# Optimization experiments

Hardware: AMD Instinct MI355X
Metric: run time of the kernel (lower is better)

## Reference

```python
import jax, jax.numpy as jnp
import numpy as np

PI = float(np.pi)
BN_EPS = 1e-3
LN_EPS = 1e-5


def ssslu(x, shape, bias):
    # x * (sin(softsign(x) * shape*pi/2) + (bias + 1))
    s = x / (1.0 + jnp.abs(x))
    return x * (jnp.sin(s * (shape * PI / 2.0)) + (bias + 1.0))


def bn(x, g, b, m, v):
    inv = (g / jnp.sqrt(v + BN_EPS))[None, :, None, None]
    return (x - m[None, :, None, None]) * inv + b[None, :, None, None]


def conv2d(x, w, bias=None, pad=0):
    y = jax.lax.conv_general_dilated(x, w, (1, 1), [(pad, pad), (pad, pad)],
                                     dimension_numbers=('NCHW', 'OIHW', 'NCHW'))
    if bias is not None:
        y = y + bias[None, :, None, None]
    return y


def ln_silu(v):
    # LayerNorm (unit weight, zero bias) over last axis, then SiLU
    mu = jnp.mean(v, axis=-1, keepdims=True)
    var = jnp.mean(jnp.square(v - mu), axis=-1, keepdims=True)
    h = (v - mu) / jnp.sqrt(var + LN_EPS)
    return h * jax.nn.sigmoid(h)


def _forward(x, w_qkv, g_qkv, b_qkv, m_qkv, v_qkv,
             w_co, g_co, b_co, m_co, v_co,
             w_b1, bias_b1, g_b1, b_b1, m_b1, v_b1,
             w_b2, bias_b2, g_b2, b_b2, m_b2, v_b2):
    B, C, H, W = x.shape
    Q = (w_qkv.shape[0] - C) // 2
    # qkv Conv block: conv1x1 -> SSSLU(-3, 0.3) -> BN
    t = bn(ssslu(conv2d(x, w_qkv, pad=0), -3.0, 0.3), g_qkv, b_qkv, m_qkv, v_qkv)
    xq, xk, xv = jnp.split(t, [Q, 2 * Q], axis=1)
    # max-pooled Q/K rows and columns -> [B*Q, W] / [B*Q, H]
    qw = jnp.max(xq, axis=2).reshape(B * Q, W)
    kw = jnp.max(xk, axis=2).reshape(B * Q, W)
    qh = jnp.max(xq, axis=3).reshape(B * Q, H)
    kh = jnp.max(xk, axis=3).reshape(B * Q, H)
    # xaw[i,b] = max_a qw[i,a]*kw[i,b]; xah[i,a] = max_b qh[i,a]*kh[i,b]
    xaw = jnp.max(qw[:, :, None] * kw[:, None, :], axis=1)  # [BQ, W]
    xah = jnp.max(qh[:, :, None] * kh[:, None, :], axis=2)  # [BQ, H]
    xaw = ln_silu(xaw)
    xah = ln_silu(xah)
    xa = (xah[:, :, None] * xaw[:, None, :]).reshape(B, Q, H, W)
    # co: SSSLUConv(Q+C -> Q): conv3x3 -> BN -> SSSLU(1.0, 0)
    xa = jnp.concatenate([xa, xv], axis=1)
    xa = ssslu(bn(conv2d(xa, w_co, pad=1), g_co, b_co, m_co, v_co), 1.0, 0.0)
    # back[0]: Conv(Q -> C, k3, bias): conv -> SSSLU(-3, 0.3) -> BN
    xa = bn(ssslu(conv2d(xa, w_b1, bias_b1, pad=1), -3.0, 0.3), g_b1, b_b1, m_b1, v_b1)
    # back[1]: SSSLUConv(C -> C, k1, bias): conv -> BN -> SSSLU(0.8, 0)
    xa = ssslu(bn(conv2d(xa, w_b2, bias_b2, pad=0), g_b2, b_b2, m_b2, v_b2), 0.8, 0.0)
    # back[2]: Sigmoid; source returns the gate itself
    return jax.nn.sigmoid(xa)


def setup_inputs() -> dict:
    B, C, Q, H, W = 16, 256, 256, 64, 64
    key = jax.random.key(0)
    ks = jax.random.split(key, 32)

    def w_init(k, o, i, kh, kw):
        return jax.random.normal(k, (o, i, kh, kw), jnp.float32) * (1.0 / np.sqrt(i * kh * kw))

    def bn_params(k, c):
        k1, k2, k3, k4 = jax.random.split(k, 4)
        g = jax.random.uniform(k1, (c,), jnp.float32, 0.5, 1.5)
        b = jax.random.normal(k2, (c,), jnp.float32) * 0.1
        m = jax.random.normal(k3, (c,), jnp.float32) * 0.1
        v = jax.random.uniform(k4, (c,), jnp.float32, 0.5, 1.5)
        return g, b, m, v

    x = jax.random.normal(ks[0], (B, C, H, W), jnp.float32)
    w_qkv = w_init(ks[1], 2 * Q + C, C, 1, 1)
    g_qkv, b_qkv, m_qkv, v_qkv = bn_params(ks[2], 2 * Q + C)
    w_co = w_init(ks[3], Q, Q + C, 3, 3)
    g_co, b_co, m_co, v_co = bn_params(ks[4], Q)
    w_b1 = w_init(ks[5], C, Q, 3, 3)
    bias_b1 = jax.random.normal(ks[6], (C,), jnp.float32) * 0.05
    g_b1, b_b1, m_b1, v_b1 = bn_params(ks[7], C)
    w_b2 = w_init(ks[8], C, C, 1, 1)
    bias_b2 = jax.random.normal(ks[9], (C,), jnp.float32) * 0.05
    g_b2, b_b2, m_b2, v_b2 = bn_params(ks[10], C)
    return dict(x=x, w_qkv=w_qkv, g_qkv=g_qkv, b_qkv=b_qkv, m_qkv=m_qkv, v_qkv=v_qkv,
                w_co=w_co, g_co=g_co, b_co=b_co, m_co=m_co, v_co=v_co,
                w_b1=w_b1, bias_b1=bias_b1, g_b1=g_b1, b_b1=b_b1, m_b1=m_b1, v_b1=v_b1,
                w_b2=w_b2, bias_b2=bias_b2, g_b2=g_b2, b_b2=b_b2, m_b2=m_b2, v_b2=v_b2)


def reference(x, w_qkv, g_qkv, b_qkv, m_qkv, v_qkv,
              w_co, g_co, b_co, m_co, v_co,
              w_b1, bias_b1, g_b1, b_b1, m_b1, v_b1,
              w_b2, bias_b2, g_b2, b_b2, m_b2, v_b2):
    return _forward(x, w_qkv, g_qkv, b_qkv, m_qkv, v_qkv,
                    w_co, g_co, b_co, m_co, v_co,
                    w_b1, bias_b1, g_b1, b_b1, m_b1, v_b1,
                    w_b2, bias_b2, g_b2, b_b2, m_b2, v_b2)
```

## Files before the change

kernel.cpp:

```cpp
#include <hip/hip_runtime.h>
#include <hip/hip_bf16.h>
#include <math.h>

#define PI_F 3.14159265358979323846f

typedef unsigned short u16;
typedef unsigned int   u32;
typedef float    f32x4 __attribute__((ext_vector_type(4)));
typedef _Float16 f16x8 __attribute__((ext_vector_type(8)));
typedef u16      u16x8 __attribute__((ext_vector_type(8)));
typedef u16      u16x4 __attribute__((ext_vector_type(4)));

__device__ __forceinline__ u16 f2h(float f){ union{ _Float16 h; u16 u; } c; c.h = (_Float16)f; return c.u; }
__device__ __forceinline__ float h2f(u16 u){ union{ u16 u; _Float16 h; } c; c.u = u; return (float)c.h; }

__device__ __forceinline__ void gl16(const void* g, void* l){
  __builtin_amdgcn_global_load_lds((const __attribute__((address_space(1))) u32*)g,
                                   (__attribute__((address_space(3))) u32*)l, 16, 0, 0);
}

__device__ __forceinline__ int SWZ(int r){ return (r>>1)&3; }

__device__ __forceinline__ float wred_max(float v){
#pragma unroll
  for (int m = 32; m; m >>= 1) v = fmaxf(v, __shfl_xor(v, m));
  return v;
}
__device__ __forceinline__ float wred_min(float v){
#pragma unroll
  for (int m = 32; m; m >>= 1) v = fminf(v, __shfl_xor(v, m));
  return v;
}
__device__ __forceinline__ float wred_sum(float v){
#pragma unroll
  for (int m = 32; m; m >>= 1) v += __shfl_xor(v, m);
  return v;
}

__device__ __forceinline__ float ssslu_f(float x, float shp, float bp1){
  float s = x / (1.0f + fabsf(x));
  return x * (__sinf(s * shp) + bp1);
}

__device__ __forceinline__ float epi_val(float v, float4 p, float shp, float bp1, int ORDER, bool SIG){
  v += p.w;
  if (ORDER == 0){ v = ssslu_f(v, shp, bp1); v = (v - p.z) * p.x + p.y; }
  else           { v = (v - p.z) * p.x + p.y; v = ssslu_f(v, shp, bp1); }
  if (SIG) v = 1.f / (1.f + __expf(-v));
  return v;
}

__device__ __forceinline__ f16x8 mul8h(u16x8 a, u16x8 b){
  union{ u16x8 u; f16x8 h; } A, B; A.u = a; B.u = b;
  return A.h * B.h;
}

__global__ __launch_bounds__(256)
void xpose_k(const float* __restrict__ X, u16* __restrict__ XH)
{
  __shared__ u16 L[16384];
  const int tid = threadIdx.x;
  const int b = blockIdx.x >> 6, h = blockIdx.x & 63;
  const float* xp = X + (size_t)b * 256 * 4096 + h * 64;
#pragma unroll
  for (int i = 0; i < 16; ++i){
    int ci = i * 16 + (tid >> 4);
    int w4 = (tid & 15) * 4;
    float4 v = *(const float4*)(xp + (size_t)ci * 4096 + w4);
    int sw = 4 * ((ci >> 3) & 15);
    u16x4 d;
    d[0] = f2h(v.x); d[1] = f2h(v.y); d[2] = f2h(v.z); d[3] = f2h(v.w);
    *(u16x4*)&L[ci * 64 + (w4 ^ sw)] = d;
  }
  __syncthreads();
  u16* out = XH + (((size_t)b * 4096 + (size_t)h * 64) << 8);
#pragma unroll
  for (int it = 0; it < 8; ++it){
    int w   = it * 8 + (tid >> 5);
    int m   = tid & 31;
    int ci0 = m * 8;
    int base = (w & ~3) ^ (4 * (m & 15));
    int wl   = w & 3;
    u16x8 o;
#pragma unroll
    for (int k = 0; k < 8; ++k)
      o[k] = L[(ci0 + k) * 64 + base + wl];
    *(u16x8*)&out[w * 256 + ci0] = o;
  }
}

template<int CI_T, bool CAT>
__global__ __launch_bounds__(256, 2)
void conv3_mfma(const u16* __restrict__ Apk, const u16* __restrict__ Bg,
                u16* __restrict__ DstH, const float4* __restrict__ pp,
                const u16* __restrict__ xahT_, const u16* __restrict__ xawT_,
                float shp, float bp1, int ORDER)
{
  constexpr int NCC = CI_T / 32;
  constexpr int NIT = NCC * 3;
  __shared__ __align__(16) u16 sAB[37248];

  const int tid  = threadIdx.x;
  const int lane = tid & 63;
  const int wv   = tid >> 6;
  const int wn   = wv;
  const int l15  = lane & 15, l4 = lane >> 4;

  const int bx  = blockIdx.x;
  const int bid = (bx & 7) * 32 + (bx >> 3);
  const int b   = bid >> 4;
  const int r0  = (bid & 15) * 4;
  const int m0  = blockIdx.y * 128;

  if (tid < 192){
    int rr = tid >> 5, rem = tid & 31;
    int wp = (rem & 16) ? 65 : 0;
    *(u32*)&sAB[24576 + rr * 2112 + wp * 32 + (rem & 15) * 2] = 0;
  }
  if (r0 == 0)
    for (int i = tid; i < 1056; i += 256) *(u32*)&sAB[24576 + i * 2] = 0;
  if (r0 == 60)
    for (int i = tid; i < 1056; i += 256) *(u32*)&sAB[24576 + 5 * 2112 + i * 2] = 0;

  const int rA = tid >> 2, s4 = tid & 3;
  const u32 offA0 = ((u32)rA * CI_T + ((s4 ^ SWZ(rA)) << 3)) * 2;
  const u32 offA1 = ((u32)(rA + 64) * CI_T + ((s4 ^ SWZ(rA + 64)) << 3)) * 2;
  const u32 offB  = (((u32)rA << 8) + ((s4 ^ SWZ(rA + 1)) << 3)) * 2;

  auto STAGE_A = [&](int it2){
    int d2 = it2 % 3, c2 = it2 / 3;
    u16* dst = &sAB[(it2 & 1) * 12288 + wv * 512];
    const char* pa = (const char*)(Apk + ((size_t)(d2 * 3 * 256) + m0) * CI_T + c2 * 32);
#pragma unroll
    for (int j2 = 0; j2 < 3; ++j2){
      gl16(pa + offA0, dst + j2 * 4096);
      gl16(pa + offA1, dst + j2 * 4096 + 2048);
      pa += (size_t)256 * CI_T * 2;
    }
  };
  auto STAGE_B = [&](int c2){
#pragma unroll
    for (int j = 0; j < 6; ++j){
      int hh = r0 - 1 + j;
      if ((unsigned)hh >= 64u) continue;
      if (CAT && c2 < 8){
        int w = rA, s = s4;
        int ci0 = c2 * 32 + ((s ^ SWZ(w + 1)) << 3);
        u16x8 vh = *(const u16x8*)&xahT_[((b * 64 + hh) << 8) + ci0];
        u16x8 vw = *(const u16x8*)&xawT_[((b * 64 + w ) << 8) + ci0];
        *(f16x8*)&sAB[24576 + j * 2112 + (w + 1) * 32 + s * 8] = mul8h(vh, vw);
      } else {
        int cio = CAT ? (c2 * 32 - 256) : (c2 * 32);
        const char* pb = (const char*)(Bg + (((size_t)b * 4096 + (size_t)hh * 64) << 8) + cio);
        gl16(pb + offB, &sAB[24576 + j * 2112 + 32 + wv * 512]);
      }
    }
  };

  f32x4 acc[8][4];
#pragma unroll
  for (int i = 0; i < 8; ++i)
#pragma unroll
    for (int j = 0; j < 4; ++j){ acc[i][j][0]=0.f; acc[i][j][1]=0.f; acc[i][j][2]=0.f; acc[i][j][3]=0.f; }

  const char* lds = (const char*)sAB;
  const u32 aoff = (u32)l15 * 64 + (u32)((l4 ^ ((l15 >> 1) & 3)) << 4);
  const char* ab0 = lds + aoff;
  const char* ab1 = lds + aoff + 24576;
  const u32 bcom = 49152u + (u32)wn * 4224;
  const char* bb0 = lds + bcom + (u32)(l15 + 0) * 64 + (u32)((l4 ^ (((l15 + 0) >> 1) & 3)) << 4);
  const char* bb1 = lds + bcom + (u32)(l15 + 1) * 64 + (u32)((l4 ^ (((l15 + 1) >> 1) & 3)) << 4);
  const char* bb2 = lds + bcom + (u32)(l15 + 2) * 64 + (u32)((l4 ^ (((l15 + 2) >> 1) & 3)) << 4);

  STAGE_A(0);

  for (int c = 0; c < NCC; ++c){
#pragma unroll
    for (int d = 0; d < 3; ++d){
      const int it = 3 * c + d;
      if (it + 1 < NIT) STAGE_A(it + 1);
      if (d == 0){ STAGE_B(c); __syncthreads(); }

      const char* ab = ((c + d) & 1) ? ab1 : ab0;
#pragma unroll
      for (int dw = 0; dw < 3; ++dw){
        const char* bp = (dw == 0) ? bb0 : (dw == 1) ? bb1 : bb2;
        f16x8 afr[8], bfr[4];
#pragma unroll
        for (int fm = 0; fm < 8; ++fm)
          afr[fm] = *(const f16x8*)(ab + dw * 8192 + fm * 1024);
#pragma unroll
        for (int fn = 0; fn < 4; ++fn)
          bfr[fn] = *(const f16x8*)(bp + d * 4224 + fn * 1024);
        __builtin_amdgcn_s_setprio(1);
#pragma unroll
        for (int fm = 0; fm < 8; ++fm)
#pragma unroll
          for (int fn = 0; fn < 4; ++fn)
            acc[fm][fn] = __builtin_amdgcn_mfma_f32_16x16x32_f16(afr[fm], bfr[fn], acc[fm][fn], 0, 0, 0);
        __builtin_amdgcn_s_setprio(0);
      }
      __syncthreads();
    }
  }

  const int h = r0 + wn;
#pragma unroll
  for (int fm = 0; fm < 8; ++fm){
    const int cobase = m0 + fm * 16 + 4 * l4;
    float4 P0 = pp[cobase], P1 = pp[cobase+1], P2 = pp[cobase+2], P3 = pp[cobase+3];
#pragma unroll
    for (int fn = 0; fn < 4; ++fn){
      int w = fn * 16 + l15;
      float v0 = epi_val(acc[fm][fn][0], P0, shp, bp1, ORDER, false);
      float v1 = epi_val(acc[fm][fn][1], P1, shp, bp1, ORDER, false);
      float v2 = epi_val(acc[fm][fn][2], P2, shp, bp1, ORDER, false);
      float v3 = epi_val(acc[fm][fn][3], P3, shp, bp1, ORDER, false);
      uint2 st;
      st.x = (u32)f2h(v0) | ((u32)f2h(v1) << 16);
      st.y = (u32)f2h(v2) | ((u32)f2h(v3) << 16);
      *(uint2*)&DstH[(((size_t)b * 4096 + (size_t)h * 64 + w) << 8) + cobase] = st;
    }
  }
}

template<int EPI>
__global__ __launch_bounds__(512, 2)
void conv1_big(const u16* __restrict__ Apk, const u16* __restrict__ Bg,
               u16* __restrict__ DstH, float* __restrict__ DstF,
               const float4* __restrict__ pp,
               float shp, float bp1, int ORDER)
{
  __shared__ __align__(16) u16 sA[2][8192];
  __shared__ __align__(16) u16 sB[2][8192];

  const int tid  = threadIdx.x;
  const int lane = tid & 63;
  const int wv   = tid >> 6;
  const int wm   = wv >> 2;
  const int wn   = wv & 3;
  const int l15  = lane & 15, l4 = lane >> 4;

  const int bx  = blockIdx.x;
  const int bid = (bx & 7) * 32 + (bx >> 3);
  const int b   = bid >> 4;
  const int h0  = (bid & 15) * 4;

  auto STAGE = [&](int c){
    int buf = c & 1;
#pragma unroll
    for (int j = 0; j < 2; ++j){
      int g = j * 512 + tid;
      int m = g >> 2, s = g & 3;
      const u16* srcA = Apk + (size_t)m * 256 + c * 32 + ((s ^ SWZ(m)) << 3);
      gl16(srcA, &sA[buf][(j * 512 + wv * 64) * 8]);
      int r = g >> 8, w = (g >> 2) & 63;
      const u16* srcB = Bg + (((size_t)b * 4096 + (h0 + r) * 64 + w) << 8) + c * 32 + ((s ^ SWZ(w)) << 3);
      gl16(srcB, &sB[buf][(j * 512 + wv * 64) * 8]);
    }
  };

  f32x4 acc[8][4];
#pragma unroll
  for (int i = 0; i < 8; ++i)
#pragma unroll
    for (int j = 0; j < 4; ++j){ acc[i][j][0]=0.f; acc[i][j][1]=0.f; acc[i][j][2]=0.f; acc[i][j][3]=0.f; }

  STAGE(0);
  __syncthreads();

  for (int c = 0; c < 8; ++c){
    if (c + 1 < 8) STAGE(c + 1);
    const int buf = c & 1;
    f16x8 afr[8], bfr[4];
#pragma unroll
    for (int fm = 0; fm < 8; ++fm){
      int m  = wm * 128 + fm * 16 + l15;
      int sl = l4 ^ SWZ(m);
      afr[fm] = *(const f16x8*)&sA[buf][m * 32 + sl * 8];
    }
#pragma unroll
    for (int fn = 0; fn < 4; ++fn){
      int w  = fn * 16 + l15;
      int sl = l4 ^ SWZ(w);
      bfr[fn] = *(const f16x8*)&sB[buf][(wn * 64 + w) * 32 + sl * 8];
    }
    __builtin_amdgcn_s_setprio(1);
#pragma unroll
    for (int fm = 0; fm < 8; ++fm)
#pragma unroll
      for (int fn = 0; fn < 4; ++fn)
        acc[fm][fn] = __builtin_amdgcn_mfma_f32_16x16x32_f16(afr[fm], bfr[fn], acc[fm][fn], 0, 0, 0);
    __builtin_amdgcn_s_setprio(0);
    __syncthreads();
  }

  const int h = h0 + wn;
#pragma unroll
  for (int fm = 0; fm < 8; ++fm){
    const int cobase = wm * 128 + fm * 16 + 4 * l4;
    float4 P0 = pp[cobase], P1 = pp[cobase+1], P2 = pp[cobase+2], P3 = pp[cobase+3];
#pragma unroll
    for (int fn = 0; fn < 4; ++fn){
      int w = fn * 16 + l15;
      if (EPI == 1){
        float v0 = epi_val(acc[fm][fn][0], P0, shp, bp1, ORDER, false);
        float v1 = epi_val(acc[fm][fn][1], P1, shp, bp1, ORDER, false);
        float v2 = epi_val(acc[fm][fn][2], P2, shp, bp1, ORDER, false);
        float v3 = epi_val(acc[fm][fn][3], P3, shp, bp1, ORDER, false);
        uint2 st;
        st.x = (u32)f2h(v0) | ((u32)f2h(v1) << 16);
        st.y = (u32)f2h(v2) | ((u32)f2h(v3) << 16);
        *(uint2*)&DstH[(((size_t)b * 4096 + (size_t)h * 64 + w) << 8) + cobase] = st;
      } else {
        float v0 = epi_val(acc[fm][fn][0], P0, shp, bp1, ORDER, true);
        float v1 = epi_val(acc[fm][fn][1], P1, shp, bp1, ORDER, true);
        float v2 = epi_val(acc[fm][fn][2], P2, shp, bp1, ORDER, true);
        float v3 = epi_val(acc[fm][fn][3], P3, shp, bp1, ORDER, true);
        size_t base = ((size_t)(b * 256 + cobase)) * 4096 + (size_t)h * 64 + w;
        DstF[base]          = v0;
        DstF[base + 4096]   = v1;
        DstF[base + 2*4096] = v2;
        DstF[base + 3*4096] = v3;
      }
    }
  }
}

__global__ __launch_bounds__(512, 2)
void conv1_pool(const u16* __restrict__ Apk0, const u16* __restrict__ Bg,
                const float4* __restrict__ pp0,
                float* __restrict__ qhp, float* __restrict__ khp,
                float* __restrict__ qwp, float* __restrict__ kwp,
                float shp, float bp1)
{
  __shared__ __align__(16) u16 S[32768];
  u16*   sA   = S;
  u16*   sB   = S + 16384;
  float* pool = (float*)S;

  const int tid  = threadIdx.x;
  const int lane = tid & 63;
  const int wv   = tid >> 6;
  const int wm   = wv >> 2;
  const int wn   = wv & 3;
  const int l15  = lane & 15, l4 = lane >> 4;

  const int bx   = blockIdx.x;
  const int bid  = (bx & 7) * 32 + (bx >> 3);
  const int b    = bid >> 4;
  const int hblk = bid & 15;
  const int h0   = hblk * 4;
  const int m0   = blockIdx.y * 256;

  const u16*    Apk = Apk0 + (size_t)m0 * 256;
  const float4* pp  = pp0 + m0;
  float* rowp = (blockIdx.y == 0) ? qhp : khp;
  float* colp = (blockIdx.y == 0) ? qwp : kwp;

  auto STAGE = [&](int c){
    int buf = c & 1;
#pragma unroll
    for (int j = 0; j < 2; ++j){
      int g = j * 512 + tid;
      int m = g >> 2, s = g & 3;
      const u16* srcA = Apk + (size_t)m * 256 + c * 32 + ((s ^ SWZ(m)) << 3);
      gl16(srcA, &sA[buf * 8192 + (j * 512 + wv * 64) * 8]);
      int r = g >> 8, w = (g >> 2) & 63;
      const u16* srcB = Bg + (((size_t)b * 4096 + (h0 + r) * 64 + w) << 8) + c * 32 + ((s ^ SWZ(w)) << 3);
      gl16(srcB, &sB[buf * 8192 + (j * 512 + wv * 64) * 8]);
    }
  };

  f32x4 acc[8][4];
#pragma unroll
  for (int i = 0; i < 8; ++i)
#pragma unroll
    for (int j = 0; j < 4; ++j){ acc[i][j][0]=0.f; acc[i][j][1]=0.f; acc[i][j][2]=0.f; acc[i][j][3]=0.f; }

  STAGE(0);
  __syncthreads();

  for (int c = 0; c < 8; ++c){
    if (c + 1 < 8) STAGE(c + 1);
    const int buf = c & 1;
    f16x8 afr[8], bfr[4];
#pragma unroll
    for (int fm = 0; fm < 8; ++fm){
      int m  = wm * 128 + fm * 16 + l15;
      int sl = l4 ^ SWZ(m);
      afr[fm] = *(const f16x8*)&sA[buf * 8192 + m * 32 + sl * 8];
    }
#pragma unroll
    for (int fn = 0; fn < 4; ++fn){
      int w  = fn * 16 + l15;
      int sl = l4 ^ SWZ(w);
      bfr[fn] = *(const f16x8*)&sB[buf * 8192 + (wn * 64 + w) * 32 + sl * 8];
    }
    __builtin_amdgcn_s_setprio(1);
#pragma unroll
    for (int fm = 0; fm < 8; ++fm)
#pragma unroll
      for (int fn = 0; fn < 4; ++fn)
        acc[fm][fn] = __builtin_amdgcn_mfma_f32_16x16x32_f16(afr[fm], bfr[fn], acc[fm][fn], 0, 0, 0);
    __builtin_amdgcn_s_setprio(0);
    __syncthreads();
  }

  const int h = h0 + wn;
#pragma unroll
  for (int k = 0; k < 4; ++k){
    if (wn == k){
#pragma unroll
      for (int fm = 0; fm < 8; ++fm){
        const int cl = wm * 128 + fm * 16 + 4 * l4;
        float4 P0 = pp[cl], P1 = pp[cl+1], P2 = pp[cl+2], P3 = pp[cl+3];
        float ev[4][4];
#pragma unroll
        for (int fn = 0; fn < 4; ++fn){
          ev[fn][0] = epi_val(acc[fm][fn][0], P0, shp, bp1, 0, false);
          ev[fn][1] = epi_val(acc[fm][fn][1], P1, shp, bp1, 0, false);
          ev[fn][2] = epi_val(acc[fm][fn][2], P2, shp, bp1, 0, false);
          ev[fn][3] = epi_val(acc[fm][fn][3], P3, shp, bp1, 0, false);
        }
#pragma unroll
        for (int r = 0; r < 4; ++r){
          float mv = fmaxf(fmaxf(ev[0][r], ev[1][r]), fmaxf(ev[2][r], ev[3][r]));
          mv = fmaxf(mv, __shfl_xor(mv, 1));
          mv = fmaxf(mv, __shfl_xor(mv, 2));
          mv = fmaxf(mv, __shfl_xor(mv, 4));
          mv = fmaxf(mv, __shfl_xor(mv, 8));
          if (l15 == 0)
            rowp[(((b << 8) | (cl + r)) << 6) + h] = mv;
        }
#pragma unroll
        for (int fn = 0; fn < 4; ++fn)
#pragma unroll
          for (int r = 0; r < 4; ++r){
            int idx = ((cl + r) << 6) + fn * 16 + l15;
            pool[idx] = (k == 0) ? ev[fn][r] : fmaxf(pool[idx], ev[fn][r]);
          }
      }
    }
    __syncthreads();
  }
  float* cbase = colp + (((size_t)(b * 16 + hblk)) << 14);
#pragma unroll
  for (int j = 0; j < 8; ++j){
    int fi = j * 512 + tid;
    *(float4*)&cbase[fi * 4] = *(const float4*)&pool[fi * 4];
  }
}

__device__ __forceinline__ float ln_silu_wave(float v){
  float mu = wred_sum(v) * (1.f / 64.f);
  float d = v - mu;
  float var = wred_sum(d * d) * (1.f / 64.f);
  float hn = d * rsqrtf(var + 1e-5f);
  return hn / (1.f + __expf(-hn));
}

__global__ void attn_k(const float* __restrict__ qwp, const float* __restrict__ kwp,
                       const float* __restrict__ qh, const float* __restrict__ kh,
                       u16* __restrict__ xahT, u16* __restrict__ xawT)
{
  int row  = blockIdx.x * 4 + (threadIdx.x >> 6);
  int lane = threadIdx.x & 63;
  int idx  = (row << 6) + lane;
  int b = row >> 8, q = row & 255;
  size_t pb = ((size_t)b << 18) + (q << 6) + lane;
  float qwv = -3.0e38f, kwv = -3.0e38f;
#pragma unroll
  for (int hb = 0; hb < 16; ++hb){
    qwv = fmaxf(qwv, qwp[pb + ((size_t)hb << 14)]);
    kwv = fmaxf(kwv, kwp[pb + ((size_t)hb << 14)]);
  }
  float qhv = qh[idx], khv = kh[idx];
  float Pq = wred_max(qwv), mq = wred_min(qwv);
  float Pk = wred_max(khv), mk = wred_min(khv);
  float aw = fmaxf(kwv * Pq, kwv * mq);
  float ah = fmaxf(qhv * Pk, qhv * mk);
  aw = ln_silu_wave(aw);
  ah = ln_silu_wave(ah);
  xawT[((b * 64 + lane) << 8) + q] = f2h(aw);
  xahT[((b * 64 + lane) << 8) + q] = f2h(ah);
}

__global__ void pack_k(const float* __restrict__ wqkv, const float* __restrict__ wco,
                       const float* __restrict__ wb1, const float* __restrict__ wb2,
                       const float* gq, const float* bq, const float* mq, const float* vq,
                       const float* gc, const float* bc, const float* mc, const float* vc,
                       const float* g1, const float* b1, const float* m1, const float* v1, const float* bias1,
                       const float* g2, const float* b2, const float* m2, const float* v2, const float* bias2,
                       u16* __restrict__ WQ, u16* __restrict__ WCO, u16* __restrict__ WB1, u16* __restrict__ WB2,
                       float4* __restrict__ PP)
{
  const int E0 = 196608, E1 = 196608 + 1179648, E2 = 196608 + 1179648 + 589824, E3 = 2031616;
  int i = blockIdx.x * 256 + threadIdx.x;
  if (i >= E3 + 1536) return;
  if (i < E0){ WQ[i] = f2h(wqkv[i]); }
  else if (i < E1){
    int d = i - E0; int tap = d / 131072; int rm = d % 131072; int m = rm >> 9; int ci = rm & 511;
    WCO[d] = f2h(wco[(size_t)((m << 9) | ci) * 9 + tap]);
  } else if (i < E2){
    int d = i - E1; int tap = d / 65536; int rm = d & 65535; int m = rm >> 8; int ci = rm & 255;
    WB1[d] = f2h(wb1[(size_t)((m << 8) | ci) * 9 + tap]);
  } else if (i < E3){
    int d = i - E2; WB2[d] = f2h(wb2[d]);
  } else {
    int c = i - E3;
    float g, be, mm, vv, bi;
    if (c < 768){ g = gq[c]; be = bq[c]; mm = mq[c]; vv = vq[c]; bi = 0.f; }
    else if (c < 1024){ int j = c - 768;  g = gc[j]; be = bc[j]; mm = mc[j]; vv = vc[j]; bi = 0.f; }
    else if (c < 1280){ int j = c - 1024; g = g1[j]; be = b1[j]; mm = m1[j]; vv = v1[j]; bi = bias1[j]; }
    else              { int j = c - 1280; g = g2[j]; be = b2[j]; mm = m2[j]; vv = v2[j]; bi = bias2[j]; }
    PP[c] = make_float4(g / sqrtf(vv + 1e-3f), be, mm, bi);
  }
}

extern "C" void kernel_launch(void* const* d_in, const int* in_sizes, int n_in,
                              void* d_out, int out_size, void* d_ws, size_t ws_size,
                              hipStream_t stream)
{
  const float* x       = (const float*)d_in[0];
  const float* w_qkv   = (const float*)d_in[1];
  const float* g_qkv   = (const float*)d_in[2];
  const float* b_qkv   = (const float*)d_in[3];
  const float* m_qkv   = (const float*)d_in[4];
  const float* v_qkv   = (const float*)d_in[5];
  const float* w_co    = (const float*)d_in[6];
  const float* g_co    = (const float*)d_in[7];
  const float* b_co    = (const float*)d_in[8];
  const float* m_co    = (const float*)d_in[9];
  const float* v_co    = (const float*)d_in[10];
  const float* w_b1    = (const float*)d_in[11];
  const float* bias_b1 = (const float*)d_in[12];
  const float* g_b1    = (const float*)d_in[13];
  const float* b_b1    = (const float*)d_in[14];
  const float* m_b1    = (const float*)d_in[15];
  const float* v_b1    = (const float*)d_in[16];
  const float* w_b2    = (const float*)d_in[17];
  const float* bias_b2 = (const float*)d_in[18];
  const float* g_b2    = (const float*)d_in[19];
  const float* b_b2    = (const float*)d_in[20];
  const float* m_b2    = (const float*)d_in[21];
  const float* v_b2    = (const float*)d_in[22];
  float* out = (float*)d_out;

  char* W = (char*)d_ws;
  u16*    WQ   = (u16*)(W + 0);
  u16*    WCO  = (u16*)(W + 393216);
  u16*    WB1  = (u16*)(W + 2752512);
  u16*    WB2  = (u16*)(W + 3932160);
  float4* PP   = (float4*)(W + 4063232);
  float*  qwp_ = (float*)(W + 4087808);
  float*  kwp_ = (float*)(W + 20865024);
  u16*    TV   = (u16*)(W + 4087808);
  u16*    XAHT = (u16*)(W + 37642240);
  u16*    XAWT = (u16*)(W + 38166528);
  u16*    XH   = (u16*)(W + 38690816);
  u16*    Y1   = (u16*)(W + 38690816);
  u16*    Y2   = TV;
  float*  qh_  = (float*)(W + 72245248);
  float*  kh_  = (float*)(W + 73293824);

  const size_t NEED = 74342400;
  if (ws_size < NEED) return;

  const float SHP_N3 = -3.0f * PI_F * 0.5f;
  const float SHP_1  =  1.0f * PI_F * 0.5f;
  const float SHP_08 =  0.8f * PI_F * 0.5f;

  dim3 blk(256);

  pack_k<<<7942, blk, 0, stream>>>(w_qkv, w_co, w_b1, w_b2,
      g_qkv, b_qkv, m_qkv, v_qkv,
      g_co,  b_co,  m_co,  v_co,
      g_b1,  b_b1,  m_b1,  v_b1,  bias_b1,
      g_b2,  b_b2,  m_b2,  v_b2,  bias_b2,
      WQ, WCO, WB1, WB2, PP);

  xpose_k<<<1024, blk, 0, stream>>>(x, XH);

  conv1_pool<<<dim3(256, 2), 512, 0, stream>>>(
      WQ, XH, PP, qh_, kh_, qwp_, kwp_, SHP_N3, 1.3f);

  attn_k<<<1024, blk, 0, stream>>>(qwp_, kwp_, qh_, kh_, XAHT, XAWT);

  conv1_big<1><<<256, 512, 0, stream>>>(
      WQ + (size_t)512 * 256, XH, TV, nullptr, PP + 512, SHP_N3, 1.3f, 0);

  conv3_mfma<512, true><<<dim3(256, 2), blk, 0, stream>>>(
      WCO, TV, Y1, PP + 768, XAHT, XAWT, SHP_1, 1.0f, 1);

  conv3_mfma<256, false><<<dim3(256, 2), blk, 0, stream>>>(
      WB1, Y1, Y2, PP + 1024, nullptr, nullptr, SHP_N3, 1.3f, 0);

  conv1_big<2><<<256, 512, 0, stream>>>(
      WB2, Y2, nullptr, out, PP + 1280, SHP_08, 1.0f, 1);
}
```

Baseline: 433.8 us.

## Keep full weight tile resident in LDS and stream activations straight to registers

Merges the 1x1-conv GEMM kernels into one templated kernel. It loads the whole 256x256 weight slice into 128KB of LDS once, up front, and reads activation fragments directly from global memory into registers with one-step prefetch. This removes the per-chunk double-buffered LDS staging and the per-iteration barriers. In exchange, LDS use rises to 128KB, which likely cuts occupancy to one block per CU, and B reads from global are uncoalesced fragment loads.

```diff
diff --git a/kernel.cpp b/kernel.cpp
--- a/kernel.cpp
+++ b/kernel.cpp
@@ -226,13 +226,15 @@
 
 template<int EPI>
 __global__ __launch_bounds__(512, 2)
-void conv1_big(const u16* __restrict__ Apk, const u16* __restrict__ Bg,
+void conv1_res(const u16* __restrict__ Apk0, const u16* __restrict__ Bg,
                u16* __restrict__ DstH, float* __restrict__ DstF,
-               const float4* __restrict__ pp,
+               const float4* __restrict__ pp0,
+               float* __restrict__ qhp, float* __restrict__ khp,
+               float* __restrict__ qwp, float* __restrict__ kwp,
                float shp, float bp1, int ORDER)
 {
-  __shared__ __align__(16) u16 sA[2][8192];
-  __shared__ __align__(16) u16 sB[2][8192];
+  __shared__ __align__(16) u16 AL[65536];
+  float* pool = (float*)AL;
 
   const int tid  = threadIdx.x;
   const int lane = tid & 63;
@@ -241,136 +243,33 @@
   const int wn   = wv & 3;
   const int l15  = lane & 15, l4 = lane >> 4;
 
-  const int bx  = blockIdx.x;
-  const int bid = (bx & 7) * 32 + (bx >> 3);
-  const int b   = bid >> 4;
-  const int h0  = (bid & 15) * 4;
-
-  auto STAGE = [&](int c){
-    int buf = c & 1;
-#pragma unroll
-    for (int j = 0; j < 2; ++j){
-      int g = j * 512 + tid;
-      int m = g >> 2, s = g & 3;
-      const u16* srcA = Apk + (size_t)m * 256 + c * 32 + ((s ^ SWZ(m)) << 3);
-      gl16(srcA, &sA[buf][(j * 512 + wv * 64) * 8]);
-      int r = g >> 8, w = (g >> 2) & 63;
-      const u16* srcB = Bg + (((size_t)b * 4096 + (h0 + r) * 64 + w) << 8) + c * 32 + ((s ^ SWZ(w)) << 3);
-      gl16(srcB, &sB[buf][(j * 512 + wv * 64) * 8]);
-    }
-  };
-
-  f32x4 acc[8][4];
-#pragma unroll
-  for (int i = 0; i < 8; ++i)
-#pragma unroll
-    for (int j = 0; j < 4; ++j){ acc[i][j][0]=0.f; acc[i][j][1]=0.f; acc[i][j][2]=0.f; acc[i][j][3]=0.f; }
-
-  STAGE(0);
-  __syncthreads();
-
-  for (int c = 0; c < 8; ++c){
-    if (c + 1 < 8) STAGE(c + 1);
-    const int buf = c & 1;
-    f16x8 afr[8], bfr[4];
-#pragma unroll
-    for (int fm = 0; fm < 8; ++fm){
-      int m  = wm * 128 + fm * 16 + l15;
-      int sl = l4 ^ SWZ(m);
-      afr[fm] = *(const f16x8*)&sA[buf][m * 32 + sl * 8];
-    }
-#pragma unroll
-    for (int fn = 0; fn < 4; ++fn){
-      int w  = fn * 16 + l15;
-      int sl = l4 ^ SWZ(w);
-      bfr[fn] = *(const f16x8*)&sB[buf][(wn * 64 + w) * 32 + sl * 8];
-    }
-    __builtin_amdgcn_s_setprio(1);
-#pragma unroll
-    for (int fm = 0; fm < 8; ++fm)
-#pragma unroll
-      for (int fn = 0; fn < 4; ++fn)
-        acc[fm][fn] = __builtin_amdgcn_mfma_f32_16x16x32_f16(afr[fm], bfr[fn], acc[fm][fn], 0, 0, 0);
-    __builtin_amdgcn_s_setprio(0);
-    __syncthreads();
-  }
-
-  const int h = h0 + wn;
-#pragma unroll
-  for (int fm = 0; fm < 8; ++fm){
-    const int cobase = wm * 128 + fm * 16 + 4 * l4;
-    float4 P0 = pp[cobase], P1 = pp[cobase+1], P2 = pp[cobase+2], P3 = pp[cobase+3];
-#pragma unroll
-    for (int fn = 0; fn < 4; ++fn){
-      int w = fn * 16 + l15;
-      if (EPI == 1){
-        float v0 = epi_val(acc[fm][fn][0], P0, shp, bp1, ORDER, false);
-        float v1 = epi_val(acc[fm][fn][1], P1, shp, bp1, ORDER, false);
-        float v2 = epi_val(acc[fm][fn][2], P2, shp, bp1, ORDER, false);
-        float v3 = epi_val(acc[fm][fn][3], P3, shp, bp1, ORDER, false);
-        uint2 st;
-        st.x = (u32)f2h(v0) | ((u32)f2h(v1) << 16);
-        st.y = (u32)f2h(v2) | ((u32)f2h(v3) << 16);
-        *(uint2*)&DstH[(((size_t)b * 4096 + (size_t)h * 64 + w) << 8) + cobase] = st;
-      } else {
-        float v0 = epi_val(acc[fm][fn][0], P0, shp, bp1, ORDER, true);
-        float v1 = epi_val(acc[fm][fn][1], P1, shp, bp1, ORDER, true);
-        float v2 = epi_val(acc[fm][fn][2], P2, shp, bp1, ORDER, true);
-        float v3 = epi_val(acc[fm][fn][3], P3, shp, bp1, ORDER, true);
-        size_t base = ((size_t)(b * 256 + cobase)) * 4096 + (size_t)h * 64 + w;
-        DstF[base]          = v0;
-        DstF[base + 4096]   = v1;
-        DstF[base + 2*4096] = v2;
-        DstF[base + 3*4096] = v3;
-      }
-    }
-  }
-}
-
-__global__ __launch_bounds__(512, 2)
-void conv1_pool(const u16* __restrict__ Apk0, const u16* __restrict__ Bg,
-                const float4* __restrict__ pp0,
-                float* __restrict__ qhp, float* __restrict__ khp,
-                float* __restrict__ qwp, float* __restrict__ kwp,
-                float shp, float bp1)
-{
-  __shared__ __align__(16) u16 S[32768];
-  u16*   sA   = S;
-  u16*   sB   = S + 16384;
-  float* pool = (float*)S;
-
-  const int tid  = threadIdx.x;
-  const int lane = tid & 63;
-  const int wv   = tid >> 6;
-  const int wm   = wv >> 2;
-  const int wn   = wv & 3;
-  const int l15  = lane & 15, l4 = lane >> 4;
-
   const int bx   = blockIdx.x;
   const int bid  = (bx & 7) * 32 + (bx >> 3);
   const int b    = bid >> 4;
   const int hblk = bid & 15;
   const int h0   = hblk * 4;
-  const int m0   = blockIdx.y * 256;
+  const int m0   = (EPI == 0) ? (blockIdx.y * 256) : 0;
 
   const u16*    Apk = Apk0 + (size_t)m0 * 256;
   const float4* pp  = pp0 + m0;
-  float* rowp = (blockIdx.y == 0) ? qhp : khp;
-  float* colp = (blockIdx.y == 0) ? qwp : kwp;
-
-  auto STAGE = [&](int c){
-    int buf = c & 1;
-#pragma unroll
-    for (int j = 0; j < 2; ++j){
-      int g = j * 512 + tid;
-      int m = g >> 2, s = g & 3;
-      const u16* srcA = Apk + (size_t)m * 256 + c * 32 + ((s ^ SWZ(m)) << 3);
-      gl16(srcA, &sA[buf * 8192 + (j * 512 + wv * 64) * 8]);
-      int r = g >> 8, w = (g >> 2) & 63;
-      const u16* srcB = Bg + (((size_t)b * 4096 + (h0 + r) * 64 + w) << 8) + c * 32 + ((s ^ SWZ(w)) << 3);
-      gl16(srcB, &sB[buf * 8192 + (j * 512 + wv * 64) * 8]);
-    }
-  };
+
+  {
+    const int g0 = tid;
+    const int g1 = 512 + tid;
+    const int mA0 = g0 >> 2, sA0 = g0 & 3;
+    const int mA1 = g1 >> 2, sA1 = g1 & 3;
+    const u32 offA0 = ((u32)mA0 * 256 + ((sA0 ^ SWZ(mA0)) << 3)) * 2;
+    const u32 offA1 = ((u32)mA1 * 256 + ((sA1 ^ SWZ(mA1)) << 3)) * 2;
+#pragma unroll
+    for (int c = 0; c < 8; ++c){
+      const char* pa = (const char*)(Apk + c * 32);
+      gl16(pa + offA0, &AL[c * 8192 + (wv * 64) * 8]);
+      gl16(pa + offA1, &AL[c * 8192 + (512 + wv * 64) * 8]);
+    }
+  }
+
+  const u16* Bp = Bg + (((size_t)b * 4096 + (size_t)(h0 + wn) * 64) << 8) + (l15 << 8) + (l4 << 3);
+#define LDB(c, fn) (*(const f16x8*)(Bp + ((fn) * 16 << 8) + (c) * 32))
 
   f32x4 acc[8][4];
 #pragma unroll
@@ -378,77 +277,112 @@
 #pragma unroll
     for (int j = 0; j < 4; ++j){ acc[i][j][0]=0.f; acc[i][j][1]=0.f; acc[i][j][2]=0.f; acc[i][j][3]=0.f; }
 
-  STAGE(0);
+  f16x8 bn0 = LDB(0, 0), bn1 = LDB(0, 1), bn2 = LDB(0, 2), bn3 = LDB(0, 3);
+
   __syncthreads();
 
+  const char* abase = (const char*)AL + wm * 8192 + l15 * 64 + ((l4 ^ SWZ(l15)) << 4);
+
+#pragma unroll
   for (int c = 0; c < 8; ++c){
-    if (c + 1 < 8) STAGE(c + 1);
-    const int buf = c & 1;
-    f16x8 afr[8], bfr[4];
+    f16x8 b0 = bn0, b1 = bn1, b2 = bn2, b3 = bn3;
+    if (c < 7){
+      bn0 = LDB(c + 1, 0); bn1 = LDB(c + 1, 1); bn2 = LDB(c + 1, 2); bn3 = LDB(c + 1, 3);
+    }
+    f16x8 afr[8];
+#pragma unroll
+    for (int fm = 0; fm < 8; ++fm)
+      afr[fm] = *(const f16x8*)(abase + c * 16384 + fm * 1024);
+    __builtin_amdgcn_s_setprio(1);
 #pragma unroll
     for (int fm = 0; fm < 8; ++fm){
-      int m  = wm * 128 + fm * 16 + l15;
-      int sl = l4 ^ SWZ(m);
-      afr[fm] = *(const f16x8*)&sA[buf * 8192 + m * 32 + sl * 8];
-    }
-#pragma unroll
-    for (int fn = 0; fn < 4; ++fn){
-      int w  = fn * 16 + l15;
-      int sl = l4 ^ SWZ(w);
-      bfr[fn] = *(const f16x8*)&sB[buf * 8192 + (wn * 64 + w) * 32 + sl * 8];
-    }
-    __builtin_amdgcn_s_setprio(1);
-#pragma unroll
-    for (int fm = 0; fm < 8; ++fm)
-#pragma unroll
-      for (int fn = 0; fn < 4; ++fn)
-        acc[fm][fn] = __builtin_amdgcn_mfma_f32_16x16x32_f16(afr[fm], bfr[fn], acc[fm][fn], 0, 0, 0);
+      acc[fm][0] = __builtin_amdgcn_mfma_f32_16x16x32_f16(afr[fm], b0, acc[fm][0], 0, 0, 0);
+      acc[fm][1] = __builtin_amdgcn_mfma_f32_16x16x32_f16(afr[fm], b1, acc[fm][1], 0, 0, 0);
+      acc[fm][2] = __builtin_amdgcn_mfma_f32_16x16x32_f16(afr[fm], b2, acc[fm][2], 0, 0, 0);
+      acc[fm][3] = __builtin_amdgcn_mfma_f32_16x16x32_f16(afr[fm], b3, acc[fm][3], 0, 0, 0);
+    }
     __builtin_amdgcn_s_setprio(0);
+  }
+#undef LDB
+
+  const int h = h0 + wn;
+
+  if (EPI == 0){
+    float* rowp = (blockIdx.y == 0) ? qhp : khp;
+    float* colp = (blockIdx.y == 0) ? qwp : kwp;
     __syncthreads();
-  }
-
-  const int h = h0 + wn;
-#pragma unroll
-  for (int k = 0; k < 4; ++k){
-    if (wn == k){
-#pragma unroll
-      for (int fm = 0; fm < 8; ++fm){
-        const int cl = wm * 128 + fm * 16 + 4 * l4;
-        float4 P0 = pp[cl], P1 = pp[cl+1], P2 = pp[cl+2], P3 = pp[cl+3];
-        float ev[4][4];
-#pragma unroll
-        for (int fn = 0; fn < 4; ++fn){
-          ev[fn][0] = epi_val(acc[fm][fn][0], P0, shp, bp1, 0, false);
-          ev[fn][1] = epi_val(acc[fm][fn][1], P1, shp, bp1, 0, false);
-          ev[fn][2] = epi_val(acc[fm][fn][2], P2, shp, bp1, 0, false);
-          ev[fn][3] = epi_val(acc[fm][fn][3], P3, shp, bp1, 0, false);
+#pragma unroll
+    for (int k = 0; k < 4; ++k){
+      if (wn == k){
+#pragma unroll
+        for (int fm = 0; fm < 8; ++fm){
+          const int cl = wm * 128 + fm * 16 + 4 * l4;
+          float4 P0 = pp[cl], P1 = pp[cl+1], P2 = pp[cl+2], P3 = pp[cl+3];
+          float ev[4][4];
+#pragma unroll
+          for (int fn = 0; fn < 4; ++fn){
+            ev[fn][0] = epi_val(acc[fm][fn][0], P0, shp, bp1, 0, false);
+            ev[fn][1] = epi_val(acc[fm][fn][1], P1, shp, bp1, 0, false);
+            ev[fn][2] = epi_val(acc[fm][fn][2], P2, shp, bp1, 0, false);
+            ev[fn][3] = epi_val(acc[fm][fn][3], P3, shp, bp1, 0, false);
+          }
+#pragma unroll
+          for (int r = 0; r < 4; ++r){
+            float mv = fmaxf(fmaxf(ev[0][r], ev[1][r]), fmaxf(ev[2][r], ev[3][r]));
+            mv = fmaxf(mv, __shfl_xor(mv, 1));
+            mv = fmaxf(mv, __shfl_xor(mv, 2));
+            mv = fmaxf(mv, __shfl_xor(mv, 4));
+            mv = fmaxf(mv, __shfl_xor(mv, 8));
+            if (l15 == 0)
+              rowp[(((b << 8) | (cl + r)) << 6) + h] = mv;
+          }
+#pragma unroll
+          for (int fn = 0; fn < 4; ++fn)
+#pragma unroll
+            for (int r = 0; r < 4; ++r){
+              int idx = ((cl + r) << 6) + fn * 16 + l15;
+              pool[idx] = (k == 0) ? ev[fn][r] : fmaxf(pool[idx], ev[fn][r]);
+            }
         }
-#pragma unroll
-        for (int r = 0; r < 4; ++r){
-          float mv = fmaxf(fmaxf(ev[0][r], ev[1][r]), fmaxf(ev[2][r], ev[3][r]));
-          mv = fmaxf(mv, __shfl_xor(mv, 1));
-          mv = fmaxf(mv, __shfl_xor(mv, 2));
-          mv = fmaxf(mv, __shfl_xor(mv, 4));
-          mv = fmaxf(mv, __shfl_xor(mv, 8));
-          if (l15 == 0)
-            rowp[(((b << 8) | (cl + r)) << 6) + h] = mv;
+      }
+      __syncthreads();
+    }
+    float* cbase = colp + (((size_t)(b * 16 + hblk)) << 14);
+#pragma unroll
+    for (int j = 0; j < 8; ++j){
+      int fi = j * 512 + tid;
+      *(float4*)&cbase[fi * 4] = *(const float4*)&pool[fi * 4];
+    }
+  } else {
+#pragma unroll
+    for (int fm = 0; fm < 8; ++fm){
+      const int cobase = wm * 128 + fm * 16 + 4 * l4;
+      float4 P0 = pp[cobase], P1 = pp[cobase+1], P2 = pp[cobase+2], P3 = pp[cobase+3];
+#pragma unroll
+      for (int fn = 0; fn < 4; ++fn){
+        int w = fn * 16 + l15;
+        if (EPI == 1){
+          float v0 = epi_val(acc[fm][fn][0], P0, shp, bp1, ORDER, false);
+          float v1 = epi_val(acc[fm][fn][1], P1, shp, bp1, ORDER, false);
+          float v2 = epi_val(acc[fm][fn][2], P2, shp, bp1, ORDER, false);
+          float v3 = epi_val(acc[fm][fn][3], P3, shp, bp1, ORDER, false);
+          uint2 st;
+          st.x = (u32)f2h(v0) | ((u32)f2h(v1) << 16);
+          st.y = (u32)f2h(v2) | ((u32)f2h(v3) << 16);
+          *(uint2*)&DstH[(((size_t)b * 4096 + (size_t)h * 64 + w) << 8) + cobase] = st;
+        } else {
+          float v0 = epi_val(acc[fm][fn][0], P0, shp, bp1, ORDER, true);
+          float v1 = epi_val(acc[fm][fn][1], P1, shp, bp1, ORDER, true);
+          float v2 = epi_val(acc[fm][fn][2], P2, shp, bp1, ORDER, true);
+          float v3 = epi_val(acc[fm][fn][3], P3, shp, bp1, ORDER, true);
+          size_t base = ((size_t)(b * 256 + cobase)) * 4096 + (size_t)h * 64 + w;
+          DstF[base]          = v0;
+          DstF[base + 4096]   = v1;
+          DstF[base + 2*4096] = v2;
+          DstF[base + 3*4096] = v3;
         }
-#pragma unroll
-        for (int fn = 0; fn < 4; ++fn)
-#pragma unroll
-          for (int r = 0; r < 4; ++r){
-            int idx = ((cl + r) << 6) + fn * 16 + l15;
-            pool[idx] = (k == 0) ? ev[fn][r] : fmaxf(pool[idx], ev[fn][r]);
-          }
       }
     }
-    __syncthreads();
-  }
-  float* cbase = colp + (((size_t)(b * 16 + hblk)) << 14);
-#pragma unroll
-  for (int j = 0; j < 8; ++j){
-    int fi = j * 512 + tid;
-    *(float4*)&cbase[fi * 4] = *(const float4*)&pool[fi * 4];
   }
 }
 
@@ -582,13 +516,14 @@
 
   xpose_k<<<1024, blk, 0, stream>>>(x, XH);
 
-  conv1_pool<<<dim3(256, 2), 512, 0, stream>>>(
-      WQ, XH, PP, qh_, kh_, qwp_, kwp_, SHP_N3, 1.3f);
+  conv1_res<0><<<dim3(256, 2), 512, 0, stream>>>(
+      WQ, XH, nullptr, nullptr, PP, qh_, kh_, qwp_, kwp_, SHP_N3, 1.3f, 0);
 
   attn_k<<<1024, blk, 0, stream>>>(qwp_, kwp_, qh_, kh_, XAHT, XAWT);
 
-  conv1_big<1><<<256, 512, 0, stream>>>(
-      WQ + (size_t)512 * 256, XH, TV, nullptr, PP + 512, SHP_N3, 1.3f, 0);
+  conv1_res<1><<<dim3(256, 1), 512, 0, stream>>>(
+      WQ + (size_t)512 * 256, XH, TV, nullptr, PP + 512,
+      nullptr, nullptr, nullptr, nullptr, SHP_N3, 1.3f, 0);
 
   conv3_mfma<512, true><<<dim3(256, 2), blk, 0, stream>>>(
       WCO, TV, Y1, PP + 768, XAHT, XAWT, SHP_1, 1.0f, 1);
@@ -596,6 +531,7 @@
   conv3_mfma<256, false><<<dim3(256, 2), blk, 0, stream>>>(
       WB1, Y1, Y2, PP + 1024, nullptr, nullptr, SHP_N3, 1.3f, 0);
 
-  conv1_big<2><<<256, 512, 0, stream>>>(
-      WB2, Y2, nullptr, out, PP + 1280, SHP_08, 1.0f, 1);
-}
+  conv1_res<2><<<dim3(256, 1), 512, 0, stream>>>(
+      WB2, Y2, nullptr, out, PP + 1280,
+      nullptr, nullptr, nullptr, nullptr, SHP_08, 1.0f, 1);
+}
```

Result: no change. 439.6 us (+1.3%).
